# Kernel optimization log

Hardware: AMD Instinct MI355X
Metric: run time of the kernel (lower is better)

The kernel has to match this reference:

```python
import jax, jax.numpy as jnp
import numpy as np

DIM = 768
HEADS = 12
HEAD_DIM = DIM // HEADS
B, S = 2, 2048
EPS = 1e-5


def _layernorm(x, w, b):
    mu = jnp.mean(x, axis=-1, keepdims=True)
    var = jnp.mean(jnp.square(x - mu), axis=-1, keepdims=True)
    return (x - mu) * jax.lax.rsqrt(var + EPS) * w + b


def setup_inputs() -> dict:
    key = jax.random.key(0)
    ks = jax.random.split(key, 16)
    sc = 1.0 / np.sqrt(DIM)
    inp = {
        'x': jax.random.normal(ks[0], (B, S, DIM), jnp.float32),
        'bias': jax.random.normal(ks[1], (HEADS, B, S, S), jnp.float32),
        'mask': jax.random.randint(ks[2], (1, B, S, S), 0, 2, jnp.int32),
        'ln1_w': jnp.ones((DIM,), jnp.float32),
        'ln1_b': jnp.zeros((DIM,), jnp.float32),
        'wq': jax.random.normal(ks[3], (DIM, DIM), jnp.float32) * sc,
        'bq': jnp.zeros((DIM,), jnp.float32),
        'wk': jax.random.normal(ks[4], (DIM, DIM), jnp.float32) * sc,
        'bk': jnp.zeros((DIM,), jnp.float32),
        'wv': jax.random.normal(ks[5], (DIM, DIM), jnp.float32) * sc,
        'bv': jnp.zeros((DIM,), jnp.float32),
        'wo': jax.random.normal(ks[6], (DIM, DIM), jnp.float32) * sc,
        'bo': jnp.zeros((DIM,), jnp.float32),
        'ln2_w': jnp.ones((DIM,), jnp.float32),
        'ln2_b': jnp.zeros((DIM,), jnp.float32),
        'w1': jax.random.normal(ks[7], (DIM, DIM), jnp.float32) * sc,
        'b1': jnp.zeros((DIM,), jnp.float32),
        'w2': jax.random.normal(ks[8], (DIM, DIM), jnp.float32) * sc,
        'b2': jnp.zeros((DIM,), jnp.float32),
    }
    return inp


def _split_heads(t):
    # [B,S,D] -> [H,B,S,Dh]  (matches torch view + permute(2,0,1,3))
    return t.reshape(B, S, HEADS, HEAD_DIM).transpose(2, 0, 1, 3)


def reference(x, bias, mask, ln1_w, ln1_b, wq, bq, wk, bk, wv, bv, wo, bo,
              ln2_w, ln2_b, w1, b1, w2, b2):
    xn = _layernorm(x, ln1_w, ln1_b)
    q = _split_heads(xn @ wq + bq)
    k = _split_heads(xn @ wk + bk)
    v = _split_heads(xn @ wv + bv)
    # scores: [H,B,Sq,Sk]; bias added BEFORE scaling, then masked, then scaled softmax
    scores = jnp.einsum('hbqd,hbkd->hbqk', q, k) + bias
    scores = jnp.where(mask == 0, jnp.float32(-1e20), scores)
    probs = jax.nn.softmax(scores / np.sqrt(HEAD_DIM), axis=-1)
    attn = jnp.einsum('hbqk,hbkd->hbqd', probs, v)
    attn = attn.transpose(1, 2, 0, 3).reshape(B, S, DIM)
    x = x + (attn @ wo + bo)
    xn = _layernorm(x, ln2_w, ln2_b)
    h = jax.nn.relu(xn @ w1 + b1)
    x = x + (h @ w2 + b2)
    return x
```

## Files before the change

kernel.cpp:

```cpp
#include <hip/hip_runtime.h>
#include <math.h>

#define DIMM 768
#define SEQ 2048
#define BATB 2
#define NHEAD 12
#define DHEAD 64
#define ROWS 4096

typedef __attribute__((ext_vector_type(8))) short bf16x8;
typedef __attribute__((ext_vector_type(4))) float f32x4;
typedef unsigned short ushort_t;
typedef unsigned int uint_t;

union U16 { int4 i; ushort_t u[8]; };

__device__ __forceinline__ ushort_t f2b(float f) {
    uint_t u = __float_as_uint(f);
    return (ushort_t)((u + 0x7FFFu + ((u >> 16) & 1u)) >> 16);
}

struct WPtrs { const float* s[6]; };

__global__ __launch_bounds__(256) void wtrans_k(WPtrs wp, ushort_t* __restrict__ dst)
{
    __shared__ float T[64][65];
    int wi = blockIdx.z;
    const float* in = wp.s[wi];
    ushort_t* out = dst + (size_t)wi * (DIMM * DIMM);
    int kb = blockIdx.y * 64, nb = blockIdx.x * 64;
    int t = threadIdx.x;
    int kl = t >> 4, nl = (t & 15) * 4;
    #pragma unroll
    for (int it = 0; it < 4; it++) {
        float4 a = *(const float4*)&in[(size_t)(kb + kl + it * 16) * DIMM + nb + nl];
        T[kl + it * 16][nl + 0] = a.x;
        T[kl + it * 16][nl + 1] = a.y;
        T[kl + it * 16][nl + 2] = a.z;
        T[kl + it * 16][nl + 3] = a.w;
    }
    __syncthreads();
    int no = t >> 2, ko = (t & 3) * 16;
    #pragma unroll
    for (int j = 0; j < 2; j++) {
        U16 u;
        #pragma unroll
        for (int c = 0; c < 8; c++) u.u[c] = f2b(T[ko + j * 8 + c][no]);
        *(int4*)&out[(size_t)(nb + no) * DIMM + kb + ko + j * 8] = u.i;
    }
}

__global__ __launch_bounds__(256) void ln_k(const float* __restrict__ x,
                                            const float* __restrict__ w,
                                            const float* __restrict__ b,
                                            ushort_t* __restrict__ out)
{
    int row = blockIdx.x;
    int tid = threadIdx.x;
    const float* xr = x + (size_t)row * DIMM;
    float v0 = xr[tid], v1 = xr[tid + 256], v2 = xr[tid + 512];
    float s  = v0 + v1 + v2;
    float ss = v0 * v0 + v1 * v1 + v2 * v2;
    #pragma unroll
    for (int off = 32; off > 0; off >>= 1) {
        s  += __shfl_down(s,  off);
        ss += __shfl_down(ss, off);
    }
    __shared__ float ws_[4], wss_[4];
    __shared__ float mu_s, rs_s;
    int lane = tid & 63, wid = tid >> 6;
    if (lane == 0) { ws_[wid] = s; wss_[wid] = ss; }
    __syncthreads();
    if (tid == 0) {
        float S1 = ws_[0] + ws_[1] + ws_[2] + ws_[3];
        float S2 = wss_[0] + wss_[1] + wss_[2] + wss_[3];
        float m = S1 * (1.0f / DIMM);
        float var = S2 * (1.0f / DIMM) - m * m;
        mu_s = m;
        rs_s = rsqrtf(var + 1e-5f);
    }
    __syncthreads();
    float mu = mu_s, rs = rs_s;
    ushort_t* orow = out + (size_t)row * DIMM;
    orow[tid]       = f2b((v0 - mu) * rs * w[tid]       + b[tid]);
    orow[tid + 256] = f2b((v1 - mu) * rs * w[tid + 256] + b[tid + 256]);
    orow[tid + 512] = f2b((v2 - mu) * rs * w[tid + 512] + b[tid + 512]);
}

template<int ASRC, int OMODE, bool RELU, bool RES>
__global__ __launch_bounds__(256) void mgemm_k(const ushort_t* __restrict__ A,
                                               const ushort_t* __restrict__ BT,
                                               const float* __restrict__ bias,
                                               const float* __restrict__ res,
                                               void* __restrict__ outv)
{
    __shared__ alignas(16) ushort_t Asl[8 * 64 * 8];
    __shared__ alignas(16) ushort_t Bsl[8 * 64 * 8];
    int tid = threadIdx.x;
    int lane = tid & 63, w = tid >> 6;
    int colBase = blockIdx.x * 64, rowBase = blockIdx.y * 64;

    f32x4 acc[4];
    #pragma unroll
    for (int nt = 0; nt < 4; nt++) { f32x4 z = {0.f, 0.f, 0.f, 0.f}; acc[nt] = z; }

    int sm = tid >> 2;
    int sko = (tid & 3) * 16;

    for (int kt = 0; kt < DIMM; kt += 64) {
        #pragma unroll
        for (int j = 0; j < 2; j++) {
            int k = sko + j * 8;
            size_t gidx;
            if (ASRC == 1) {
                gidx = (size_t)(rowBase + sm) * DIMM + kt + k;
            } else {
                int r = rowBase + sm, kg = kt + k;
                gidx = ((size_t)((kg >> 6) * BATB + (r >> 11)) * SEQ + (r & 2047)) * DHEAD + (kg & 63);
            }
            int4 a = *(const int4*)&A[gidx];
            int ln = (sm & 15) | (((k & 31) >> 3) << 4);
            int slot = ((sm >> 4) << 1) | (k >> 5);
            *(int4*)&Asl[(slot * 64 + ln) * 8] = a;
        }
        #pragma unroll
        for (int j = 0; j < 2; j++) {
            int k = sko + j * 8;
            int4 b = *(const int4*)&BT[(size_t)(colBase + sm) * DIMM + kt + k];
            int ln = (sm & 15) | (((k & 31) >> 3) << 4);
            int slot = (k >> 5) * 4 + (sm >> 4);
            *(int4*)&Bsl[(slot * 64 + ln) * 8] = b;
        }
        __syncthreads();
        bf16x8 a0 = *(bf16x8*)&Asl[((w * 2 + 0) * 64 + lane) * 8];
        bf16x8 a1 = *(bf16x8*)&Asl[((w * 2 + 1) * 64 + lane) * 8];
        #pragma unroll
        for (int nt = 0; nt < 4; nt++) {
            bf16x8 b0 = *(bf16x8*)&Bsl[((0 * 4 + nt) * 64 + lane) * 8];
            bf16x8 b1 = *(bf16x8*)&Bsl[((1 * 4 + nt) * 64 + lane) * 8];
            acc[nt] = __builtin_amdgcn_mfma_f32_16x16x32_bf16(a0, b0, acc[nt], 0, 0, 0);
            acc[nt] = __builtin_amdgcn_mfma_f32_16x16x32_bf16(a1, b1, acc[nt], 0, 0, 0);
        }
        __syncthreads();
    }
    int col_l = lane & 15, quad = lane >> 4;
    #pragma unroll
    for (int nt = 0; nt < 4; nt++) {
        int n = colBase + nt * 16 + col_l;
        float bn = bias[n];
        #pragma unroll
        for (int r = 0; r < 4; r++) {
            int row = rowBase + w * 16 + quad * 4 + r;
            float v = acc[nt][r] + bn;
            if (RELU) v = fmaxf(v, 0.0f);
            if (RES)  v += res[(size_t)row * DIMM + n];
            if (OMODE == 0) {
                ((float*)outv)[(size_t)row * DIMM + n] = v;
            } else if (OMODE == 1) {
                ((ushort_t*)outv)[(size_t)row * DIMM + n] = f2b(v);
            } else {
                ((ushort_t*)outv)[((size_t)((n >> 6) * BATB + (row >> 11)) * SEQ + (row & 2047)) * DHEAD + (n & 63)] = f2b(v);
            }
        }
    }
}

__global__ __launch_bounds__(256) void attn_k(const ushort_t* __restrict__ q,
                                              const ushort_t* __restrict__ k,
                                              const ushort_t* __restrict__ v,
                                              const float* __restrict__ bias,
                                              const int* __restrict__ mask,
                                              ushort_t* __restrict__ out)
{
    __shared__ alignas(16) ushort_t Kf[8 * 64 * 8];
    __shared__ alignas(16) ushort_t Vf[8 * 64 * 8];
    __shared__ alignas(16) ushort_t Pf[8 * 64 * 8];
    int tid = threadIdx.x, lane = tid & 63, w = tid >> 6;
    int col_l = lane & 15, quad = lane >> 4;
    int qbase = blockIdx.x * 64;
    int hb = blockIdx.y;
    const ushort_t* qp = q + (size_t)hb * SEQ * DHEAD;
    const ushort_t* kp = k + (size_t)hb * SEQ * DHEAD;
    const ushort_t* vp = v + (size_t)hb * SEQ * DHEAD;
    const float* bp = bias + (size_t)hb * SEQ * SEQ;
    const int*   mp = mask + (size_t)(hb & 1) * SEQ * SEQ;

    bf16x8 qF0 = *(const bf16x8*)&qp[(size_t)(qbase + w * 16 + col_l) * DHEAD + (quad * 8)];
    bf16x8 qF1 = *(const bf16x8*)&qp[(size_t)(qbase + w * 16 + col_l) * DHEAD + 32 + (quad * 8)];

    f32x4 O[4];
    #pragma unroll
    for (int nt = 0; nt < 4; nt++) { f32x4 z = {0.f, 0.f, 0.f, 0.f}; O[nt] = z; }
    float m_run[4], l_run[4];
    #pragma unroll
    for (int r = 0; r < 4; r++) { m_run[r] = -1e30f; l_run[r] = 0.0f; }

    int sn = tid >> 2, sko = (tid & 3) * 16;
    int j0 = (tid >> 3) * 2, e0 = (tid & 7) * 8;

    for (int kvb = 0; kvb < SEQ; kvb += 64) {
        #pragma unroll
        for (int jj = 0; jj < 2; jj++) {
            int kk = sko + jj * 8;
            int4 kd = *(const int4*)&kp[(size_t)(kvb + sn) * DHEAD + kk];
            int slot = (kk >> 5) * 4 + (sn >> 4);
            int ln = (sn & 15) | (((kk & 31) >> 3) << 4);
            *(int4*)&Kf[(slot * 64 + ln) * 8] = kd;
        }
        {
            U16 g0, g1;
            g0.i = *(const int4*)&vp[(size_t)(kvb + j0) * DHEAD + e0];
            g1.i = *(const int4*)&vp[(size_t)(kvb + j0 + 1) * DHEAD + e0];
            int js = j0 >> 5, grp = (j0 & 31) >> 3, i0 = j0 & 7;
            #pragma unroll
            for (int c = 0; c < 8; c++) {
                int n = e0 + c;
                uint_t pk = (uint_t)g0.u[c] | ((uint_t)g1.u[c] << 16);
                int idx = ((js * 4 + (n >> 4)) * 64 + ((n & 15) | (grp << 4))) * 8 + i0;
                *(uint_t*)&Vf[idx] = pk;
            }
        }
        float bl[4][4]; int ml[4][4];
        #pragma unroll
        for (int nt = 0; nt < 4; nt++) {
            int col = kvb + nt * 16 + col_l;
            #pragma unroll
            for (int r = 0; r < 4; r++) {
                int qrow = qbase + w * 16 + quad * 4 + r;
                bl[nt][r] = bp[(size_t)qrow * SEQ + col];
                ml[nt][r] = mp[(size_t)qrow * SEQ + col];
            }
        }
        __syncthreads();
        f32x4 S[4];
        #pragma unroll
        for (int nt = 0; nt < 4; nt++) {
            bf16x8 b0 = *(bf16x8*)&Kf[((0 * 4 + nt) * 64 + lane) * 8];
            bf16x8 b1 = *(bf16x8*)&Kf[((1 * 4 + nt) * 64 + lane) * 8];
            f32x4 z = {0.f, 0.f, 0.f, 0.f};
            z = __builtin_amdgcn_mfma_f32_16x16x32_bf16(qF0, b0, z, 0, 0, 0);
            S[nt] = __builtin_amdgcn_mfma_f32_16x16x32_bf16(qF1, b1, z, 0, 0, 0);
        }
        float lg[4][4];
        #pragma unroll
        for (int nt = 0; nt < 4; nt++)
            #pragma unroll
            for (int r = 0; r < 4; r++)
                lg[nt][r] = ml[nt][r] ? (S[nt][r] + bl[nt][r]) * 0.125f : -1.25e19f;
        float alpha[4];
        #pragma unroll
        for (int r = 0; r < 4; r++) {
            float mx = fmaxf(fmaxf(lg[0][r], lg[1][r]), fmaxf(lg[2][r], lg[3][r]));
            mx = fmaxf(mx, __shfl_xor(mx, 1));
            mx = fmaxf(mx, __shfl_xor(mx, 2));
            mx = fmaxf(mx, __shfl_xor(mx, 4));
            mx = fmaxf(mx, __shfl_xor(mx, 8));
            float mnew = fmaxf(m_run[r], mx);
            alpha[r] = __expf(m_run[r] - mnew);
            m_run[r] = mnew;
            float rs = 0.0f;
            #pragma unroll
            for (int nt = 0; nt < 4; nt++) {
                float p = __expf(lg[nt][r] - mnew);
                lg[nt][r] = p;
                rs += p;
            }
            rs += __shfl_xor(rs, 1);
            rs += __shfl_xor(rs, 2);
            rs += __shfl_xor(rs, 4);
            rs += __shfl_xor(rs, 8);
            l_run[r] = l_run[r] * alpha[r] + rs;
        }
        #pragma unroll
        for (int nt = 0; nt < 4; nt++)
            #pragma unroll
            for (int r = 0; r < 4; r++)
                O[nt][r] *= alpha[r];
        #pragma unroll
        for (int nt = 0; nt < 4; nt++) {
            int j = nt * 16 + col_l;
            #pragma unroll
            for (int r = 0; r < 4; r++) {
                ushort_t pu = f2b(lg[nt][r]);
                uint_t po = (uint_t)(unsigned)__shfl_xor((int)pu, 1);
                if ((lane & 1) == 0) {
                    int m = quad * 4 + r;
                    int idx = ((w * 2 + (j >> 5)) * 64 + (m | (((j & 31) >> 3) << 4))) * 8 + (j & 7);
                    *(uint_t*)&Pf[idx] = (uint_t)pu | (po << 16);
                }
            }
        }
        #pragma unroll
        for (int js = 0; js < 2; js++) {
            bf16x8 pF = *(bf16x8*)&Pf[((w * 2 + js) * 64 + lane) * 8];
            #pragma unroll
            for (int nt = 0; nt < 4; nt++) {
                bf16x8 vF = *(bf16x8*)&Vf[((js * 4 + nt) * 64 + lane) * 8];
                O[nt] = __builtin_amdgcn_mfma_f32_16x16x32_bf16(pF, vF, O[nt], 0, 0, 0);
            }
        }
        __syncthreads();
    }
    float inv[4];
    #pragma unroll
    for (int r = 0; r < 4; r++) inv[r] = 1.0f / l_run[r];
    #pragma unroll
    for (int nt = 0; nt < 4; nt++)
        #pragma unroll
        for (int r = 0; r < 4; r++) {
            int row = qbase + w * 16 + quad * 4 + r;
            out[((size_t)hb * SEQ + row) * DHEAD + nt * 16 + col_l] = f2b(O[nt][r] * inv[r]);
        }
}

extern "C" void kernel_launch(void* const* d_in, const int* in_sizes, int n_in,
                              void* d_out, int out_size, void* d_ws, size_t ws_size,
                              hipStream_t stream)
{
    const float* x    = (const float*)d_in[0];
    const float* bias = (const float*)d_in[1];
    const int*   mask = (const int*)d_in[2];
    const float* ln1w = (const float*)d_in[3];
    const float* ln1b = (const float*)d_in[4];
    const float* wq   = (const float*)d_in[5];
    const float* bq   = (const float*)d_in[6];
    const float* wk   = (const float*)d_in[7];
    const float* bk   = (const float*)d_in[8];
    const float* wv   = (const float*)d_in[9];
    const float* bv   = (const float*)d_in[10];
    const float* wo   = (const float*)d_in[11];
    const float* bo   = (const float*)d_in[12];
    const float* ln2w = (const float*)d_in[13];
    const float* ln2b = (const float*)d_in[14];
    const float* w1   = (const float*)d_in[15];
    const float* b1   = (const float*)d_in[16];
    const float* w2   = (const float*)d_in[17];
    const float* b2   = (const float*)d_in[18];

    const size_t WSZ = (size_t)DIMM * DIMM;
    const size_t ABUF = (size_t)ROWS * DIMM;

    ushort_t* wsu  = (ushort_t*)d_ws;
    ushort_t* wT   = wsu;
    ushort_t* qb   = wsu + 6 * WSZ;
    ushort_t* kbuf = qb + ABUF;
    ushort_t* vbuf = kbuf + ABUF;
    ushort_t* xn1  = vbuf + ABUF;
    float*    x1   = (float*)(xn1 + ABUF);
    ushort_t* hid  = qb;

    WPtrs wp; wp.s[0] = wq; wp.s[1] = wk; wp.s[2] = wv; wp.s[3] = wo; wp.s[4] = w1; wp.s[5] = w2;

    dim3 gg(12, 64), gb(256);
    wtrans_k<<<dim3(12, 12, 6), 256, 0, stream>>>(wp, wT);
    ln_k<<<ROWS, 256, 0, stream>>>(x, ln1w, ln1b, xn1);
    mgemm_k<1, 2, false, false><<<gg, gb, 0, stream>>>(xn1, wT + 0 * WSZ, bq, nullptr, qb);
    mgemm_k<1, 2, false, false><<<gg, gb, 0, stream>>>(xn1, wT + 1 * WSZ, bk, nullptr, kbuf);
    mgemm_k<1, 2, false, false><<<gg, gb, 0, stream>>>(xn1, wT + 2 * WSZ, bv, nullptr, vbuf);
    attn_k<<<dim3(32, 24), 256, 0, stream>>>(qb, kbuf, vbuf, bias, mask, xn1);
    mgemm_k<2, 0, false, true><<<gg, gb, 0, stream>>>(xn1, wT + 3 * WSZ, bo, x, x1);
    ln_k<<<ROWS, 256, 0, stream>>>(x1, ln2w, ln2b, xn1);
    mgemm_k<1, 1, true, false><<<gg, gb, 0, stream>>>(xn1, wT + 4 * WSZ, b1, nullptr, hid);
    mgemm_k<1, 0, false, true><<<gg, gb, 0, stream>>>(hid, wT + 5 * WSZ, b2, x1, (float*)d_out);
}
```

Before: 750.6 us.

## Use direct global-to-LDS loads, fuse QKV GEMMs, and lazily rescale softmax with exp2

```diff
diff --git a/kernel.cpp b/kernel.cpp
--- a/kernel.cpp
+++ b/kernel.cpp
@@ -20,7 +20,15 @@
     return (ushort_t)((u + 0x7FFFu + ((u >> 16) & 1u)) >> 16);
 }
 
+__device__ __forceinline__ void gl16(const ushort_t* g, ushort_t* l) {
+    __builtin_amdgcn_global_load_lds(
+        (const __attribute__((address_space(1))) unsigned int*)g,
+        (__attribute__((address_space(3))) unsigned int*)l,
+        16, 0, 0);
+}
+
 struct WPtrs { const float* s[6]; };
+struct BPtrs { const float* p[3]; };
 
 __global__ __launch_bounds__(256) void wtrans_k(WPtrs wp, ushort_t* __restrict__ dst)
 {
@@ -87,10 +95,10 @@
     orow[tid + 512] = f2b((v2 - mu) * rs * w[tid + 512] + b[tid + 512]);
 }
 
-template<int ASRC, int OMODE, bool RELU, bool RES>
+template<int ASRC, int OMODE, bool RELU, bool RES, int NB>
 __global__ __launch_bounds__(256) void mgemm_k(const ushort_t* __restrict__ A,
                                                const ushort_t* __restrict__ BT,
-                                               const float* __restrict__ bias,
+                                               BPtrs bias,
                                                const float* __restrict__ res,
                                                void* __restrict__ outv)
 {
@@ -100,37 +108,43 @@
     int lane = tid & 63, w = tid >> 6;
     int colBase = blockIdx.x * 64, rowBase = blockIdx.y * 64;
 
+    size_t offA[2], offB[2];
+    ushort_t* dstA[2];
+    ushort_t* dstB[2];
+    const size_t strideA = (ASRC == 1) ? (size_t)64 : (size_t)BATB * SEQ * DHEAD;
+    #pragma unroll
+    for (int i = 0; i < 2; i++) {
+        int slot = i * 4 + w;
+        {
+            int sm = ((slot >> 1) << 4) | (lane & 15);
+            int c  = ((slot & 1) << 2) | (lane >> 4);
+            if (ASRC == 1) {
+                offA[i] = (size_t)(rowBase + sm) * DIMM + 8 * c;
+            } else {
+                int r = rowBase + sm;
+                offA[i] = ((size_t)(r >> 11) * SEQ + (r & 2047)) * DHEAD + 8 * c;
+            }
+            dstA[i] = &Asl[(size_t)(i * 256 + w * 64) * 8];
+        }
+        {
+            int sm = ((slot & 3) << 4) | (lane & 15);
+            int c  = ((slot >> 2) << 2) | (lane >> 4);
+            offB[i] = (size_t)(colBase + sm) * DIMM + 8 * c;
+            dstB[i] = &Bsl[(size_t)(i * 256 + w * 64) * 8];
+        }
+    }
+
     f32x4 acc[4];
     #pragma unroll
     for (int nt = 0; nt < 4; nt++) { f32x4 z = {0.f, 0.f, 0.f, 0.f}; acc[nt] = z; }
 
-    int sm = tid >> 2;
-    int sko = (tid & 3) * 16;
-
-    for (int kt = 0; kt < DIMM; kt += 64) {
-        #pragma unroll
-        for (int j = 0; j < 2; j++) {
-            int k = sko + j * 8;
-            size_t gidx;
-            if (ASRC == 1) {
-                gidx = (size_t)(rowBase + sm) * DIMM + kt + k;
-            } else {
-                int r = rowBase + sm, kg = kt + k;
-                gidx = ((size_t)((kg >> 6) * BATB + (r >> 11)) * SEQ + (r & 2047)) * DHEAD + (kg & 63);
-            }
-            int4 a = *(const int4*)&A[gidx];
-            int ln = (sm & 15) | (((k & 31) >> 3) << 4);
-            int slot = ((sm >> 4) << 1) | (k >> 5);
-            *(int4*)&Asl[(slot * 64 + ln) * 8] = a;
-        }
-        #pragma unroll
-        for (int j = 0; j < 2; j++) {
-            int k = sko + j * 8;
-            int4 b = *(const int4*)&BT[(size_t)(colBase + sm) * DIMM + kt + k];
-            int ln = (sm & 15) | (((k & 31) >> 3) << 4);
-            int slot = (k >> 5) * 4 + (sm >> 4);
-            *(int4*)&Bsl[(slot * 64 + ln) * 8] = b;
-        }
+    for (int t = 0; t < DIMM / 64; t++) {
+        gl16(A  + offA[0], dstA[0]);
+        gl16(A  + offA[1], dstA[1]);
+        gl16(BT + offB[0], dstB[0]);
+        gl16(BT + offB[1], dstB[1]);
+        offA[0] += strideA; offA[1] += strideA;
+        offB[0] += 64;      offB[1] += 64;
         __syncthreads();
         bf16x8 a0 = *(bf16x8*)&Asl[((w * 2 + 0) * 64 + lane) * 8];
         bf16x8 a1 = *(bf16x8*)&Asl[((w * 2 + 1) * 64 + lane) * 8];
@@ -143,11 +157,14 @@
         }
         __syncthreads();
     }
+    int wi = (NB == 3) ? (int)(blockIdx.x / 12) : 0;
+    const float* bp_ = bias.p[wi];
+    int nLoc0 = colBase - wi * DIMM;
     int col_l = lane & 15, quad = lane >> 4;
     #pragma unroll
     for (int nt = 0; nt < 4; nt++) {
         int n = colBase + nt * 16 + col_l;
-        float bn = bias[n];
+        float bn = bp_[nLoc0 + nt * 16 + col_l];
         #pragma unroll
         for (int r = 0; r < 4; r++) {
             int row = rowBase + w * 16 + quad * 4 + r;
@@ -188,6 +205,17 @@
     bf16x8 qF0 = *(const bf16x8*)&qp[(size_t)(qbase + w * 16 + col_l) * DHEAD + (quad * 8)];
     bf16x8 qF1 = *(const bf16x8*)&qp[(size_t)(qbase + w * 16 + col_l) * DHEAD + 32 + (quad * 8)];
 
+    size_t offK[2];
+    ushort_t* dstK[2];
+    #pragma unroll
+    for (int i = 0; i < 2; i++) {
+        int slot = i * 4 + w;
+        int sn = ((slot & 3) << 4) | (lane & 15);
+        int c  = ((slot >> 2) << 2) | (lane >> 4);
+        offK[i] = (size_t)sn * DHEAD + 8 * c;
+        dstK[i] = &Kf[(size_t)(i * 256 + w * 64) * 8];
+    }
+
     f32x4 O[4];
     #pragma unroll
     for (int nt = 0; nt < 4; nt++) { f32x4 z = {0.f, 0.f, 0.f, 0.f}; O[nt] = z; }
@@ -195,18 +223,12 @@
     #pragma unroll
     for (int r = 0; r < 4; r++) { m_run[r] = -1e30f; l_run[r] = 0.0f; }
 
-    int sn = tid >> 2, sko = (tid & 3) * 16;
     int j0 = (tid >> 3) * 2, e0 = (tid & 7) * 8;
+    const float C2 = 0.18033688011112042f;
 
     for (int kvb = 0; kvb < SEQ; kvb += 64) {
-        #pragma unroll
-        for (int jj = 0; jj < 2; jj++) {
-            int kk = sko + jj * 8;
-            int4 kd = *(const int4*)&kp[(size_t)(kvb + sn) * DHEAD + kk];
-            int slot = (kk >> 5) * 4 + (sn >> 4);
-            int ln = (sn & 15) | (((kk & 31) >> 3) << 4);
-            *(int4*)&Kf[(slot * 64 + ln) * 8] = kd;
-        }
+        gl16(kp + (size_t)kvb * DHEAD + offK[0], dstK[0]);
+        gl16(kp + (size_t)kvb * DHEAD + offK[1], dstK[1]);
         {
             U16 g0, g1;
             g0.i = *(const int4*)&vp[(size_t)(kvb + j0) * DHEAD + e0];
@@ -246,8 +268,7 @@
         for (int nt = 0; nt < 4; nt++)
             #pragma unroll
             for (int r = 0; r < 4; r++)
-                lg[nt][r] = ml[nt][r] ? (S[nt][r] + bl[nt][r]) * 0.125f : -1.25e19f;
-        float alpha[4];
+                lg[nt][r] = ml[nt][r] ? (S[nt][r] + bl[nt][r]) * C2 : -2.0e18f;
         #pragma unroll
         for (int r = 0; r < 4; r++) {
             float mx = fmaxf(fmaxf(lg[0][r], lg[1][r]), fmaxf(lg[2][r], lg[3][r]));
@@ -255,13 +276,19 @@
             mx = fmaxf(mx, __shfl_xor(mx, 2));
             mx = fmaxf(mx, __shfl_xor(mx, 4));
             mx = fmaxf(mx, __shfl_xor(mx, 8));
-            float mnew = fmaxf(m_run[r], mx);
-            alpha[r] = __expf(m_run[r] - mnew);
-            m_run[r] = mnew;
+            if (!__all(mx - m_run[r] <= 4.0f)) {
+                float mnew = fmaxf(m_run[r], mx);
+                float alpha = __builtin_amdgcn_exp2f(m_run[r] - mnew);
+                m_run[r] = mnew;
+                l_run[r] *= alpha;
+                #pragma unroll
+                for (int nt = 0; nt < 4; nt++) O[nt][r] *= alpha;
+            }
+            float mcur = m_run[r];
             float rs = 0.0f;
             #pragma unroll
             for (int nt = 0; nt < 4; nt++) {
-                float p = __expf(lg[nt][r] - mnew);
+                float p = __builtin_amdgcn_exp2f(lg[nt][r] - mcur);
                 lg[nt][r] = p;
                 rs += p;
             }
@@ -269,13 +296,8 @@
             rs += __shfl_xor(rs, 2);
             rs += __shfl_xor(rs, 4);
             rs += __shfl_xor(rs, 8);
-            l_run[r] = l_run[r] * alpha[r] + rs;
-        }
-        #pragma unroll
-        for (int nt = 0; nt < 4; nt++)
-            #pragma unroll
-            for (int r = 0; r < 4; r++)
-                O[nt][r] *= alpha[r];
+            l_run[r] += rs;
+        }
         #pragma unroll
         for (int nt = 0; nt < 4; nt++) {
             int j = nt * 16 + col_l;
@@ -350,16 +372,18 @@
     ushort_t* hid  = qb;
 
     WPtrs wp; wp.s[0] = wq; wp.s[1] = wk; wp.s[2] = wv; wp.s[3] = wo; wp.s[4] = w1; wp.s[5] = w2;
+    BPtrs bqkv; bqkv.p[0] = bq; bqkv.p[1] = bk; bqkv.p[2] = bv;
+    BPtrs bbo;  bbo.p[0]  = bo; bbo.p[1]  = bo; bbo.p[2]  = bo;
+    BPtrs bb1;  bb1.p[0]  = b1; bb1.p[1]  = b1; bb1.p[2]  = b1;
+    BPtrs bb2;  bb2.p[0]  = b2; bb2.p[1]  = b2; bb2.p[2]  = b2;
 
     dim3 gg(12, 64), gb(256);
     wtrans_k<<<dim3(12, 12, 6), 256, 0, stream>>>(wp, wT);
     ln_k<<<ROWS, 256, 0, stream>>>(x, ln1w, ln1b, xn1);
-    mgemm_k<1, 2, false, false><<<gg, gb, 0, stream>>>(xn1, wT + 0 * WSZ, bq, nullptr, qb);
-    mgemm_k<1, 2, false, false><<<gg, gb, 0, stream>>>(xn1, wT + 1 * WSZ, bk, nullptr, kbuf);
-    mgemm_k<1, 2, false, false><<<gg, gb, 0, stream>>>(xn1, wT + 2 * WSZ, bv, nullptr, vbuf);
+    mgemm_k<1, 2, false, false, 3><<<dim3(36, 64), gb, 0, stream>>>(xn1, wT, bqkv, nullptr, qb);
     attn_k<<<dim3(32, 24), 256, 0, stream>>>(qb, kbuf, vbuf, bias, mask, xn1);
-    mgemm_k<2, 0, false, true><<<gg, gb, 0, stream>>>(xn1, wT + 3 * WSZ, bo, x, x1);
+    mgemm_k<2, 0, false, true, 1><<<gg, gb, 0, stream>>>(xn1, wT + 3 * WSZ, bbo, x, x1);
     ln_k<<<ROWS, 256, 0, stream>>>(x1, ln2w, ln2b, xn1);
-    mgemm_k<1, 1, true, false><<<gg, gb, 0, stream>>>(xn1, wT + 4 * WSZ, b1, nullptr, hid);
-    mgemm_k<1, 0, false, true><<<gg, gb, 0, stream>>>(hid, wT + 5 * WSZ, b2, x1, (float*)d_out);
-}
+    mgemm_k<1, 1, true, false, 1><<<gg, gb, 0, stream>>>(xn1, wT + 4 * WSZ, bb1, nullptr, hid);
+    mgemm_k<1, 0, false, true, 1><<<gg, gb, 0, stream>>>(hid, wT + 5 * WSZ, bb2, x1, (float*)d_out);
+}
```

Measured after the change: 783.0 us. 4.3% more time.
